# Kernel tuning notes

Measured on AMD Instinct MI355X. Metric: run time of the kernel, lower is better.

Reference implementation:

```python
import jax, jax.numpy as jnp
import numpy as np

# Grid constants derived from init kwargs: min_pt=0, max_pt=128, step=1, eps=1e-8
ORIGIN = -(1.0 + 1e-8)          # per-dim origin of control grid
STEP = 1.0
MAX_COORD = 130.0               # control_grid_size (132) - 2
PTS_N = 2_000_000
GRID = 132
CHANNELS = 1


def setup_inputs() -> dict:
    key = jax.random.key(0)
    k1, k2 = jax.random.split(key)
    # points in world coords, uniform over the interpolable domain
    pts = jax.random.uniform(k1, (PTS_N, 3), dtype=jnp.float32) * 128.0
    control_pts = jax.random.normal(k2, (CHANNELS, GRID, GRID, GRID), dtype=jnp.float32)
    return {"pts": pts, "control_pts": control_pts}


def _coefs(x):
    # Cardinal cubic B-spline basis (Irwin-Hall n=4), x in [0,1). [pts] -> [pts,4]
    omx = 1.0 - x
    c0 = omx ** 3
    c1 = 3.0 * (x - 2.0) * x ** 2 + 4.0
    c2 = -3.0 * omx ** 2 * (x + 1.0) + 4.0
    c3 = x ** 3
    return jnp.stack([c0, c1, c2, c3], axis=-1) / 6.0


def reference(pts, control_pts):
    padding_value = 0.0
    # to control-grid coordinates
    t = (pts - ORIGIN) / STEP                                   # [P,3]
    in_bounds = jnp.all(t >= 1.0, axis=-1) & jnp.all(t < MAX_COORD, axis=-1)  # [P]
    t = jnp.where(in_bounds[:, None], t, 1.0)
    ti = t.astype(jnp.int32)                                    # trunc == floor since t>=1
    frac = t - ti.astype(t.dtype)                               # [P,3]
    w = _coefs(frac.reshape(-1)).reshape(-1, 3, 4)              # [P,3,4]

    stencil = jnp.arange(-1, 3, dtype=jnp.int32)                # [-1,0,1,2]
    idx = ti[..., None] + stencil                               # [P,3,4]
    # gather the 4x4x4 control-point stencil per point: [C,P,4,4,4]
    cp = control_pts[:, idx[:, 0, :, None, None], idx[:, 1, None, :, None], idx[:, 2, None, None, :]]
    # tensor-product weighted sum
    vals = jnp.einsum('cpijk,pi,pj,pk->pc', cp, w[:, 0], w[:, 1], w[:, 2])  # [P,C]
    vals = jnp.where(in_bounds[:, None], vals, jnp.float32(padding_value))
    return vals
```

## Files before the change

### kernel.cpp

```cpp
#include <hip/hip_runtime.h>

#define GRID_DIM 132
#define SLAB (GRID_DIM * GRID_DIM)
#define NB 512
#define CHUNK 4096
#define KPT (CHUNK / 256)
#define REG 20
#define REG2 (REG * REG)
#define REG3 (REG * REG * REG)
#define STRIPE 8192

__device__ __forceinline__ void bspline_w(float x, float w[4]) {
    float omx = 1.0f - x;
    w[0] = omx * omx * omx * (1.0f / 6.0f);
    w[1] = (3.0f * (x - 2.0f) * x * x + 4.0f) * (1.0f / 6.0f);
    w[2] = (-3.0f * omx * omx * (x + 1.0f) + 4.0f) * (1.0f / 6.0f);
    w[3] = x * x * x * (1.0f / 6.0f);
}

__device__ __forceinline__ void load_pt(const float* __restrict__ pts, int i,
                                        float& tx, float& ty, float& tz, bool& inb) {
    tx = pts[3 * i + 0] + 1.0f;
    ty = pts[3 * i + 1] + 1.0f;
    tz = pts[3 * i + 2] + 1.0f;
    inb = (tx >= 1.0f) && (ty >= 1.0f) && (tz >= 1.0f) &&
          (tx < 130.0f) && (ty < 130.0f) && (tz < 130.0f);
    if (!inb) { tx = ty = tz = 1.0f; }
}

__device__ __forceinline__ int calc_bin(float tx, float ty, float tz) {
    int bx = min(7, ((int)tx - 1) >> 4);
    int by = min(7, ((int)ty - 1) >> 4);
    int bz = min(7, ((int)tz - 1) >> 4);
    return (bx << 6) | (by << 3) | bz;
}

__device__ __forceinline__ int chunk_swizzle(int bid, int nblk) {
    int q = nblk >> 3, r = nblk & 7;
    int xcd = bid & 7, pos = bid >> 3;
    return (xcd < r ? xcd * (q + 1) : r * (q + 1) + (xcd - r) * q) + pos;
}

__device__ __forceinline__ void local_stripe_scan(
    const unsigned* __restrict__ stot, int nstripe,
    unsigned* soff, unsigned* sc)
{
    int t = threadIdx.x;
    if (t < 256) sc[t] = (t < nstripe) ? stot[t] : 0u;
    __syncthreads();
    for (int off = 1; off < 256; off <<= 1) {
        unsigned v = (t >= off && t < 256) ? sc[t - off] : 0u;
        __syncthreads();
        if (t < 256) sc[t] += v;
        __syncthreads();
    }
    if (t < 256) soff[t] = (t == 0) ? 0u : sc[t - 1];
    __syncthreads();
}

__global__ __launch_bounds__(256) void hist512_kernel(
    const float* __restrict__ pts, int n, int nblk, unsigned* __restrict__ bh)
{
    __shared__ unsigned lh[NB];
    int tid = threadIdx.x, blk = blockIdx.x;
    int c0 = blk * CHUNK;
    for (int b = tid; b < NB; b += 256) lh[b] = 0u;
    __syncthreads();
#pragma unroll
    for (int k = 0; k < KPT; ++k) {
        int i = c0 + tid + k * 256;
        if (i < n) {
            float tx, ty, tz; bool inb;
            load_pt(pts, i, tx, ty, tz, inb);
            atomicAdd(&lh[calc_bin(tx, ty, tz)], 1u);
        }
    }
    __syncthreads();
    for (int b = tid; b < NB; b += 256) bh[b * nblk + blk] = lh[b];
}

__global__ __launch_bounds__(256) void scan_l1_kernel(
    const unsigned* __restrict__ bh, unsigned* __restrict__ seg,
    unsigned* __restrict__ stot, int TOT)
{
    __shared__ unsigned sc[256];
    int t = threadIdx.x;
    int base_idx = blockIdx.x * STRIPE + t * 32;
    unsigned local[32];
    unsigned s = 0;
#pragma unroll
    for (int j = 0; j < 32; ++j) {
        int idx = base_idx + j;
        unsigned v = (idx < TOT) ? bh[idx] : 0u;
        local[j] = v; s += v;
    }
    sc[t] = s;
    __syncthreads();
    for (int off = 1; off < 256; off <<= 1) {
        unsigned v = (t >= off) ? sc[t - off] : 0u;
        __syncthreads();
        sc[t] += v;
        __syncthreads();
    }
    unsigned run = (t == 0) ? 0u : sc[t - 1];
#pragma unroll
    for (int j = 0; j < 32; ++j) {
        int idx = base_idx + j;
        if (idx < TOT) seg[idx] = run;
        run += local[j];
    }
    if (t == 255) stot[blockIdx.x] = sc[255];
}

__global__ __launch_bounds__(256) void partition_kernel(
    const float* __restrict__ pts, int n, int nblk,
    const unsigned* __restrict__ seg, const unsigned* __restrict__ stot,
    int nstripe, float4* __restrict__ sorted)
{
    __shared__ unsigned lcur[NB];
    __shared__ unsigned sc[256], soff[256];

    local_stripe_scan(stot, nstripe, soff, sc);

    int blk = chunk_swizzle(blockIdx.x, nblk);
    int tid = threadIdx.x;
    int c0 = blk * CHUNK;

    for (int b = tid; b < NB; b += 256) {
        int idx = b * nblk + blk;
        lcur[b] = seg[idx] + soff[idx >> 13];
    }
    __syncthreads();

#pragma unroll
    for (int k = 0; k < KPT; ++k) {
        int i = c0 + tid + k * 256;
        if (i < n) {
            float tx, ty, tz; bool inb;
            load_pt(pts, i, tx, ty, tz, inb);
            int bin = calc_bin(tx, ty, tz);
            unsigned g = atomicAdd(&lcur[bin], 1u);
            unsigned tag = (unsigned)i | (inb ? 0u : 0x80000000u);
            sorted[g] = make_float4(tx, ty, tz, __uint_as_float(tag));
        }
    }
}

__global__ __launch_bounds__(512) void eval_kernel(
    const float4* __restrict__ sorted, const float* __restrict__ cp,
    const unsigned* __restrict__ seg, const unsigned* __restrict__ stot,
    int nstripe, float* __restrict__ out, int n, int nblk)
{
    __shared__ float region[REG3];
    __shared__ unsigned sc[256], soff[256];

    local_stripe_scan(stot, nstripe, soff, sc);

    int bid = blockIdx.x;
    int bin = (bid & 7) * 64 + (bid >> 3);
    int x0 = (bin >> 6) << 4, y0 = ((bin >> 3) & 7) << 4, z0 = (bin & 7) << 4;

    const float* src = cp + (size_t)x0 * SLAB + y0 * GRID_DIM + z0;
    for (int v = threadIdx.x; v < REG3; v += 512) {
        int gx = v / REG2;
        int rr = v - gx * REG2;
        int gy = rr / REG;
        int gz = rr - gy * REG;
        region[v] = src[gx * SLAB + gy * GRID_DIM + gz];
    }
    __syncthreads();

    int i0 = bin * nblk;
    unsigned s = seg[i0] + soff[i0 >> 13];
    unsigned e;
    if (bin == NB - 1) e = (unsigned)n;
    else { int i1 = (bin + 1) * nblk; e = seg[i1] + soff[i1 >> 13]; }

    for (unsigned i = s + threadIdx.x; i < e; i += 512) {
        float4 p = sorted[i];
        unsigned tag = __float_as_uint(p.w);
        int ix = (int)p.x, iy = (int)p.y, iz = (int)p.z;
        float wx[4], wy[4], wz[4];
        bspline_w(p.x - (float)ix, wx);
        bspline_w(p.y - (float)iy, wy);
        bspline_w(p.z - (float)iz, wz);
        int lx = ix - 1 - x0, ly = iy - 1 - y0, lz = iz - 1 - z0;
        const float* rb = region + (lx * REG + ly) * REG + lz;
        float acc = 0.0f;
#pragma unroll
        for (int a = 0; a < 4; ++a) {
            float accy = 0.0f;
#pragma unroll
            for (int b = 0; b < 4; ++b) {
                const float* row = rb + (a * REG + b) * REG;
                float sz = fmaf(row[0], wz[0], fmaf(row[1], wz[1],
                           fmaf(row[2], wz[2], row[3] * wz[3])));
                accy = fmaf(wy[b], sz, accy);
            }
            acc = fmaf(wx[a], accy, acc);
        }
        int orig = (int)(tag & 0x7fffffffu);
        out[orig] = (tag >> 31) ? 0.0f : acc;
    }
}

__global__ __launch_bounds__(256) void eval_unsorted_kernel(
    const float* __restrict__ pts, const float* __restrict__ cp,
    float* __restrict__ out, int n)
{
    int i = blockIdx.x * blockDim.x + threadIdx.x;
    if (i >= n) return;
    float tx, ty, tz; bool inb;
    load_pt(pts, i, tx, ty, tz, inb);
    int ix = (int)tx, iy = (int)ty, iz = (int)tz;
    float wx[4], wy[4], wz[4];
    bspline_w(tx - (float)ix, wx);
    bspline_w(ty - (float)iy, wy);
    bspline_w(tz - (float)iz, wz);
    const float* bse = cp + (size_t)(ix - 1) * SLAB + (size_t)(iy - 1) * GRID_DIM + (iz - 1);
    float acc = 0.0f;
#pragma unroll
    for (int a = 0; a < 4; ++a) {
        float accy = 0.0f;
#pragma unroll
        for (int b = 0; b < 4; ++b) {
            const float* row = bse + a * SLAB + b * GRID_DIM;
            float4 v;
            __builtin_memcpy(&v, row, 16);
            float sz = fmaf(v.x, wz[0], fmaf(v.y, wz[1], fmaf(v.z, wz[2], v.w * wz[3])));
            accy = fmaf(wy[b], sz, accy);
        }
        acc = fmaf(wx[a], accy, acc);
    }
    out[i] = inb ? acc : 0.0f;
}

extern "C" void kernel_launch(void* const* d_in, const int* in_sizes, int n_in,
                              void* d_out, int out_size, void* d_ws, size_t ws_size,
                              hipStream_t stream) {
    const float* pts = (const float*)d_in[0];
    const float* cp  = (const float*)d_in[1];
    float* out       = (float*)d_out;

    int n = in_sizes[0] / 3;
    int nblk = (n + CHUNK - 1) / CHUNK;
    int TOT = NB * nblk;
    int nstripe = (TOT + STRIPE - 1) / STRIPE;

    size_t A          = (((size_t)TOT * 4) + 1023) & ~(size_t)1023;
    size_t off_seg    = A;
    size_t off_stot   = 2 * A;
    size_t off_sorted = 2 * A + 1024;
    size_t need       = off_sorted + (size_t)n * sizeof(float4);

    if (ws_size >= need && nblk <= 1024 && nstripe <= 256) {
        unsigned* bh     = (unsigned*)d_ws;
        unsigned* seg    = (unsigned*)((char*)d_ws + off_seg);
        unsigned* stot   = (unsigned*)((char*)d_ws + off_stot);
        float4*   sorted = (float4*)((char*)d_ws + off_sorted);

        hipLaunchKernelGGL(hist512_kernel, dim3(nblk), dim3(256), 0, stream,
                           pts, n, nblk, bh);
        hipLaunchKernelGGL(scan_l1_kernel, dim3(nstripe), dim3(256), 0, stream,
                           bh, seg, stot, TOT);
        hipLaunchKernelGGL(partition_kernel, dim3(nblk), dim3(256), 0, stream,
                           pts, n, nblk, seg, stot, nstripe, sorted);
        hipLaunchKernelGGL(eval_kernel, dim3(NB), dim3(512), 0, stream,
                           sorted, cp, seg, stot, nstripe, out, n, nblk);
    } else {
        hipLaunchKernelGGL(eval_unsorted_kernel, dim3((n + 255) / 256), dim3(256), 0, stream,
                           pts, cp, out, n);
    }
}
```

Measured before the change: 149.6 us.

## Fuse histogram, scan, partition and eval into one cooperative kernel

Replaces the four-kernel bin-sort pipeline with a single cooperative kernel of 1024 blocks that uses grid-wide syncs between the histogram, scan, scatter and evaluation phases. Points are kept in registers between the histogram and scatter phases, so the point array is read only once, and the eval phase splits each bin across two blocks. The goal is to remove launch gaps and the second read of the points. The cost is three grid barriers and a requirement that all 1024 blocks be co-resident. If the cooperative launch fails, the code falls back to the separate kernels.

```diff
diff --git a/kernel.cpp b/kernel.cpp
--- a/kernel.cpp
+++ b/kernel.cpp
@@ -1,14 +1,20 @@
 #include <hip/hip_runtime.h>
+#include <hip/hip_cooperative_groups.h>
+
+namespace cg = cooperative_groups;
 
 #define GRID_DIM 132
 #define SLAB (GRID_DIM * GRID_DIM)
 #define NB 512
-#define CHUNK 4096
-#define KPT (CHUNK / 256)
+#define NBLKF 1024
+#define CHUNKF 2048
+#define KPTF (CHUNKF / 256)
+#define TOTF (NB * NBLKF)
+#define STRIPE 8192
+#define NSTRIPEF (TOTF / STRIPE)
 #define REG 20
 #define REG2 (REG * REG)
 #define REG3 (REG * REG * REG)
-#define STRIPE 8192
 
 __device__ __forceinline__ void bspline_w(float x, float w[4]) {
     float omx = 1.0f - x;
@@ -35,12 +41,6 @@
     return (bx << 6) | (by << 3) | bz;
 }
 
-__device__ __forceinline__ int chunk_swizzle(int bid, int nblk) {
-    int q = nblk >> 3, r = nblk & 7;
-    int xcd = bid & 7, pos = bid >> 3;
-    return (xcd < r ? xcd * (q + 1) : r * (q + 1) + (xcd - r) * q) + pos;
-}
-
 __device__ __forceinline__ void local_stripe_scan(
     const unsigned* __restrict__ stot, int nstripe,
     unsigned* soff, unsigned* sc)
@@ -58,16 +58,142 @@
     __syncthreads();
 }
 
+__global__ __launch_bounds__(256, 4) void fused_kernel(
+    const float* __restrict__ pts, const float* __restrict__ cp,
+    float* __restrict__ out, int n,
+    unsigned* __restrict__ bh, unsigned* __restrict__ seg,
+    unsigned* __restrict__ stot, float4* __restrict__ sorted)
+{
+    __shared__ float region[REG3];
+    __shared__ unsigned lhc[NB];
+    __shared__ unsigned sc[256], soff[256];
+
+    cg::grid_group grid = cg::this_grid();
+    int tid = threadIdx.x;
+    int bid = blockIdx.x;
+    int blk = (bid & 7) * 128 + (bid >> 3);
+    int c0 = blk * CHUNKF;
+
+    for (int b = tid; b < NB; b += 256) lhc[b] = 0u;
+    __syncthreads();
+    float4 pv[KPTF];
+#pragma unroll
+    for (int k = 0; k < KPTF; ++k) {
+        int i = c0 + tid + k * 256;
+        if (i < n) {
+            float tx, ty, tz; bool inb;
+            load_pt(pts, i, tx, ty, tz, inb);
+            unsigned tag = (unsigned)i | (inb ? 0u : 0x80000000u);
+            pv[k] = make_float4(tx, ty, tz, __uint_as_float(tag));
+            atomicAdd(&lhc[calc_bin(tx, ty, tz)], 1u);
+        }
+    }
+    __syncthreads();
+    for (int b = tid; b < NB; b += 256) bh[(b << 10) | blk] = lhc[b];
+
+    grid.sync();
+
+    if (bid < NSTRIPEF) {
+        int base_idx = bid * STRIPE + tid * 32;
+        unsigned local[32];
+        unsigned s = 0;
+#pragma unroll
+        for (int j = 0; j < 32; ++j) { unsigned v = bh[base_idx + j]; local[j] = v; s += v; }
+        sc[tid] = s;
+        __syncthreads();
+        for (int off = 1; off < 256; off <<= 1) {
+            unsigned v = (tid >= off) ? sc[tid - off] : 0u;
+            __syncthreads();
+            sc[tid] += v;
+            __syncthreads();
+        }
+        unsigned run = (tid == 0) ? 0u : sc[tid - 1];
+#pragma unroll
+        for (int j = 0; j < 32; ++j) { seg[base_idx + j] = run; run += local[j]; }
+        if (tid == 255) stot[bid] = sc[255];
+    }
+
+    grid.sync();
+
+    local_stripe_scan(stot, NSTRIPEF, soff, sc);
+    for (int b = tid; b < NB; b += 256) {
+        int idx = (b << 10) | blk;
+        lhc[b] = seg[idx] + soff[idx >> 13];
+    }
+    __syncthreads();
+#pragma unroll
+    for (int k = 0; k < KPTF; ++k) {
+        int i = c0 + tid + k * 256;
+        if (i < n) {
+            int bin = calc_bin(pv[k].x, pv[k].y, pv[k].z);
+            unsigned g = atomicAdd(&lhc[bin], 1u);
+            sorted[g] = pv[k];
+        }
+    }
+
+    grid.sync();
+
+    int sub = bid & 511, half = bid >> 9;
+    int bin = (sub & 7) * 64 + (sub >> 3);
+    int x0 = (bin >> 6) << 4, y0 = ((bin >> 3) & 7) << 4, z0 = (bin & 7) << 4;
+
+    const float* src = cp + (size_t)x0 * SLAB + y0 * GRID_DIM + z0;
+    for (int v = tid; v < REG3; v += 256) {
+        int gx = v / REG2;
+        int rr = v - gx * REG2;
+        int gy = rr / REG;
+        int gz = rr - gy * REG;
+        region[v] = src[gx * SLAB + gy * GRID_DIM + gz];
+    }
+    __syncthreads();
+
+    int i0 = bin << 10;
+    unsigned s0 = seg[i0] + soff[i0 >> 13];
+    unsigned e;
+    if (bin == NB - 1) e = (unsigned)n;
+    else { int i1 = (bin + 1) << 10; e = seg[i1] + soff[i1 >> 13]; }
+    unsigned hlen = (e - s0) >> 1;
+    unsigned ia = s0 + hlen * half;
+    unsigned ib = half ? e : s0 + hlen;
+
+    for (unsigned i = ia + tid; i < ib; i += 256) {
+        float4 p = sorted[i];
+        unsigned tag = __float_as_uint(p.w);
+        int ix = (int)p.x, iy = (int)p.y, iz = (int)p.z;
+        float wx[4], wy[4], wz[4];
+        bspline_w(p.x - (float)ix, wx);
+        bspline_w(p.y - (float)iy, wy);
+        bspline_w(p.z - (float)iz, wz);
+        int lx = ix - 1 - x0, ly = iy - 1 - y0, lz = iz - 1 - z0;
+        const float* rb = region + (lx * REG + ly) * REG + lz;
+        float acc = 0.0f;
+#pragma unroll
+        for (int a = 0; a < 4; ++a) {
+            float accy = 0.0f;
+#pragma unroll
+            for (int b = 0; b < 4; ++b) {
+                const float* row = rb + (a * REG + b) * REG;
+                float sz = fmaf(row[0], wz[0], fmaf(row[1], wz[1],
+                           fmaf(row[2], wz[2], row[3] * wz[3])));
+                accy = fmaf(wy[b], sz, accy);
+            }
+            acc = fmaf(wx[a], accy, acc);
+        }
+        int orig = (int)(tag & 0x7fffffffu);
+        out[orig] = (tag >> 31) ? 0.0f : acc;
+    }
+}
+
 __global__ __launch_bounds__(256) void hist512_kernel(
-    const float* __restrict__ pts, int n, int nblk, unsigned* __restrict__ bh)
+    const float* __restrict__ pts, int n, unsigned* __restrict__ bh)
 {
     __shared__ unsigned lh[NB];
     int tid = threadIdx.x, blk = blockIdx.x;
-    int c0 = blk * CHUNK;
+    int c0 = blk * CHUNKF;
     for (int b = tid; b < NB; b += 256) lh[b] = 0u;
     __syncthreads();
 #pragma unroll
-    for (int k = 0; k < KPT; ++k) {
+    for (int k = 0; k < KPTF; ++k) {
         int i = c0 + tid + k * 256;
         if (i < n) {
             float tx, ty, tz; bool inb;
@@ -76,12 +202,12 @@
         }
     }
     __syncthreads();
-    for (int b = tid; b < NB; b += 256) bh[b * nblk + blk] = lh[b];
+    for (int b = tid; b < NB; b += 256) bh[(b << 10) | blk] = lh[b];
 }
 
 __global__ __launch_bounds__(256) void scan_l1_kernel(
     const unsigned* __restrict__ bh, unsigned* __restrict__ seg,
-    unsigned* __restrict__ stot, int TOT)
+    unsigned* __restrict__ stot)
 {
     __shared__ unsigned sc[256];
     int t = threadIdx.x;
@@ -89,11 +215,7 @@
     unsigned local[32];
     unsigned s = 0;
 #pragma unroll
-    for (int j = 0; j < 32; ++j) {
-        int idx = base_idx + j;
-        unsigned v = (idx < TOT) ? bh[idx] : 0u;
-        local[j] = v; s += v;
-    }
+    for (int j = 0; j < 32; ++j) { unsigned v = bh[base_idx + j]; local[j] = v; s += v; }
     sc[t] = s;
     __syncthreads();
     for (int off = 1; off < 256; off <<= 1) {
@@ -104,36 +226,29 @@
     }
     unsigned run = (t == 0) ? 0u : sc[t - 1];
 #pragma unroll
-    for (int j = 0; j < 32; ++j) {
-        int idx = base_idx + j;
-        if (idx < TOT) seg[idx] = run;
-        run += local[j];
-    }
+    for (int j = 0; j < 32; ++j) { seg[base_idx + j] = run; run += local[j]; }
     if (t == 255) stot[blockIdx.x] = sc[255];
 }
 
 __global__ __launch_bounds__(256) void partition_kernel(
-    const float* __restrict__ pts, int n, int nblk,
+    const float* __restrict__ pts, int n,
     const unsigned* __restrict__ seg, const unsigned* __restrict__ stot,
-    int nstripe, float4* __restrict__ sorted)
+    float4* __restrict__ sorted)
 {
     __shared__ unsigned lcur[NB];
     __shared__ unsigned sc[256], soff[256];
-
-    local_stripe_scan(stot, nstripe, soff, sc);
-
-    int blk = chunk_swizzle(blockIdx.x, nblk);
+    local_stripe_scan(stot, NSTRIPEF, soff, sc);
+    int bid = blockIdx.x;
+    int blk = (bid & 7) * 128 + (bid >> 3);
     int tid = threadIdx.x;
-    int c0 = blk * CHUNK;
-
+    int c0 = blk * CHUNKF;
     for (int b = tid; b < NB; b += 256) {
-        int idx = b * nblk + blk;
+        int idx = (b << 10) | blk;
         lcur[b] = seg[idx] + soff[idx >> 13];
     }
     __syncthreads();
-
-#pragma unroll
-    for (int k = 0; k < KPT; ++k) {
+#pragma unroll
+    for (int k = 0; k < KPTF; ++k) {
         int i = c0 + tid + k * 256;
         if (i < n) {
             float tx, ty, tz; bool inb;
@@ -149,17 +264,14 @@
 __global__ __launch_bounds__(512) void eval_kernel(
     const float4* __restrict__ sorted, const float* __restrict__ cp,
     const unsigned* __restrict__ seg, const unsigned* __restrict__ stot,
-    int nstripe, float* __restrict__ out, int n, int nblk)
+    float* __restrict__ out, int n)
 {
     __shared__ float region[REG3];
     __shared__ unsigned sc[256], soff[256];
-
-    local_stripe_scan(stot, nstripe, soff, sc);
-
+    local_stripe_scan(stot, NSTRIPEF, soff, sc);
     int bid = blockIdx.x;
     int bin = (bid & 7) * 64 + (bid >> 3);
     int x0 = (bin >> 6) << 4, y0 = ((bin >> 3) & 7) << 4, z0 = (bin & 7) << 4;
-
     const float* src = cp + (size_t)x0 * SLAB + y0 * GRID_DIM + z0;
     for (int v = threadIdx.x; v < REG3; v += 512) {
         int gx = v / REG2;
@@ -169,13 +281,11 @@
         region[v] = src[gx * SLAB + gy * GRID_DIM + gz];
     }
     __syncthreads();
-
-    int i0 = bin * nblk;
+    int i0 = bin << 10;
     unsigned s = seg[i0] + soff[i0 >> 13];
     unsigned e;
     if (bin == NB - 1) e = (unsigned)n;
-    else { int i1 = (bin + 1) * nblk; e = seg[i1] + soff[i1 >> 13]; }
-
+    else { int i1 = (bin + 1) << 10; e = seg[i1] + soff[i1 >> 13]; }
     for (unsigned i = s + threadIdx.x; i < e; i += 512) {
         float4 p = sorted[i];
         unsigned tag = __float_as_uint(p.w);
@@ -243,30 +353,33 @@
     float* out       = (float*)d_out;
 
     int n = in_sizes[0] / 3;
-    int nblk = (n + CHUNK - 1) / CHUNK;
-    int TOT = NB * nblk;
-    int nstripe = (TOT + STRIPE - 1) / STRIPE;
-
-    size_t A          = (((size_t)TOT * 4) + 1023) & ~(size_t)1023;
-    size_t off_seg    = A;
-    size_t off_stot   = 2 * A;
-    size_t off_sorted = 2 * A + 1024;
+
+    size_t off_seg    = (size_t)TOTF * 4;
+    size_t off_stot   = off_seg + (size_t)TOTF * 4;
+    size_t off_sorted = off_stot + 1024;
     size_t need       = off_sorted + (size_t)n * sizeof(float4);
 
-    if (ws_size >= need && nblk <= 1024 && nstripe <= 256) {
+    if (ws_size >= need && n <= NBLKF * CHUNKF) {
         unsigned* bh     = (unsigned*)d_ws;
         unsigned* seg    = (unsigned*)((char*)d_ws + off_seg);
         unsigned* stot   = (unsigned*)((char*)d_ws + off_stot);
         float4*   sorted = (float4*)((char*)d_ws + off_sorted);
 
-        hipLaunchKernelGGL(hist512_kernel, dim3(nblk), dim3(256), 0, stream,
-                           pts, n, nblk, bh);
-        hipLaunchKernelGGL(scan_l1_kernel, dim3(nstripe), dim3(256), 0, stream,
-                           bh, seg, stot, TOT);
-        hipLaunchKernelGGL(partition_kernel, dim3(nblk), dim3(256), 0, stream,
-                           pts, n, nblk, seg, stot, nstripe, sorted);
-        hipLaunchKernelGGL(eval_kernel, dim3(NB), dim3(512), 0, stream,
-                           sorted, cp, seg, stot, nstripe, out, n, nblk);
+        void* args[] = { (void*)&pts, (void*)&cp, (void*)&out, (void*)&n,
+                         (void*)&bh, (void*)&seg, (void*)&stot, (void*)&sorted };
+        hipError_t err = hipLaunchCooperativeKernel(
+            (const void*)fused_kernel, dim3(NBLKF), dim3(256), args, 0, stream);
+
+        if (err != hipSuccess) {
+            hipLaunchKernelGGL(hist512_kernel, dim3(NBLKF), dim3(256), 0, stream,
+                               pts, n, bh);
+            hipLaunchKernelGGL(scan_l1_kernel, dim3(NSTRIPEF), dim3(256), 0, stream,
+                               bh, seg, stot);
+            hipLaunchKernelGGL(partition_kernel, dim3(NBLKF), dim3(256), 0, stream,
+                               pts, n, seg, stot, sorted);
+            hipLaunchKernelGGL(eval_kernel, dim3(NB), dim3(512), 0, stream,
+                               sorted, cp, seg, stot, out, n);
+        }
     } else {
         hipLaunchKernelGGL(eval_unsorted_kernel, dim3((n + 255) / 256), dim3(256), 0, stream,
                            pts, cp, out, n);
```

New measurement: 497.7 us. +232.7%, slower.
